# Kernel optimization log

Measured on AMD Instinct MI355X. Metric: run time of the kernel, lower is better.

The kernel has to match this reference:

```python
import jax, jax.numpy as jnp
import numpy as np

ROWS, COLS = 6, 7


def setup_inputs() -> dict:
    key = jax.random.key(0)
    k1, k2 = jax.random.split(key)
    N = 524288
    # gravity-consistent connect-4 boards: each column filled from the bottom
    heights = jax.random.randint(k1, (N, COLS), 0, ROWS + 1)          # pieces per column
    r = jnp.arange(ROWS)[None, :, None]                               # row 0 is top
    filled = r >= (ROWS - heights)[:, None, :]                        # (N, R, C)
    signs = jnp.where(jax.random.bernoulli(k2, 0.5, (N, ROWS, COLS)), 1.0, -1.0)
    x = jnp.where(filled, signs, 0.0).astype(jnp.float32)
    return {"x": x}


def _wins_and_playable(B):
    """For board B (N,R,C) from current player's (+1) perspective, return
    playable (N,C): column not full, and win (N,C): dropping +1 there wins."""
    N = B.shape[0]
    zero = B == 0
    playable = zero[:, 0, :]                                          # (N, C) top cell empty
    rows = jnp.arange(ROWS)
    # landing row = lowest (max-index) empty row per column; -1 if full (masked later)
    land = jnp.max(jnp.where(zero, rows[None, :, None], -1), axis=1)  # (N, C)
    n_idx = jnp.arange(N)[:, None]
    cols = jnp.arange(COLS)[None, :]
    win = jnp.zeros((N, COLS), dtype=bool)
    for dr, dc in ((0, 1), (1, 0), (1, 1), (1, -1)):
        cells = []
        for k in range(-3, 4):
            if k == 0:
                cells.append(jnp.ones((N, COLS), dtype=bool))         # the placed piece itself
                continue
            rr = land + k * dr                                        # (N, C)
            cc = cols + k * dc                                        # (1, C) -> broadcast
            valid = (rr >= 0) & (rr < ROWS) & (cc >= 0) & (cc < COLS)
            v = B[n_idx, jnp.clip(rr, 0, ROWS - 1), jnp.clip(cc, 0, COLS - 1)]
            cells.append(valid & (v == 1.0))
        cells = jnp.stack(cells, axis=-1)                             # (N, C, 7) offsets -3..3
        for s in range(4):                                            # any 4 consecutive
            win = win | jnp.all(cells[..., s:s + 4], axis=-1)
    return playable, win


def reference(x):
    squeeze = x.ndim == 2
    if squeeze:
        x = x[None]
    valids = []
    for sign in (1.0, -1.0):
        playable, win = _wins_and_playable(sign * x)
        valids.append(playable & win)
    valid = jnp.concatenate(valids, axis=1)                           # (N, 2C), priority order
    first = jnp.argmax(valid, axis=1)                                 # first True in scan order
    any_v = jnp.any(valid, axis=1)
    col = first % COLS
    logits = jnp.where(any_v[:, None],
                       jnp.log(jax.nn.one_hot(col, COLS, dtype=jnp.float32) + 1e-12),
                       0.0).astype(jnp.float32)
    return logits[0] if squeeze else logits
```

## Files before the change

kernel.cpp:

```cpp
#include <hip/hip_runtime.h>
#include <stdint.h>

#define THREADS 64
#define BOARDS_PER_BLOCK 128

typedef float f32x4 __attribute__((ext_vector_type(4)));

static constexpr uint64_t colmask(int lo, int hi) {
    uint64_t m = 0;
    for (int r = 0; r < 6; ++r)
        for (int c = lo; c <= hi; ++c)
            m |= 1ull << (7 * r + c);
    return m;
}

static __device__ __forceinline__ uint64_t win_cells(uint64_t P) {
    uint64_t w = 0;
    #pragma unroll
    for (int d = 0; d < 4; ++d) {
        const int s  = (d == 0) ? 1 : (d == 1) ? 7 : (d == 2) ? 8 : 6;
        const int dc = (d == 0) ? 1 : (d == 1) ? 0 : (d == 2) ? 1 : -1;
        const uint64_t M0 = (dc == 0) ? ~0ull : (dc > 0 ? colmask(0, 3) : colmask(3, 6));
        const uint64_t M1 = (dc == 0) ? ~0ull : (dc > 0 ? colmask(1, 4) : colmask(2, 5));
        const uint64_t M2 = (dc == 0) ? ~0ull : (dc > 0 ? colmask(2, 5) : colmask(1, 4));
        const uint64_t M3 = (dc == 0) ? ~0ull : (dc > 0 ? colmask(3, 6) : colmask(0, 3));
        uint64_t r1 = P >> s, r2 = P >> (2 * s), r3 = P >> (3 * s);
        uint64_t l1 = P << s, l2 = P << (2 * s), l3 = P << (3 * s);
        uint64_t u = r1 & r2, v = l1 & l2;
        w |= (u & r3 & M0) | (u & l1 & M1) | (v & r1 & M2) | (v & l3 & M3);
    }
    return w;
}

static __device__ __forceinline__ uint32_t colfold(uint64_t v) {
    v |= v >> 21;
    v |= v >> 7;
    v |= v >> 7;
    return (uint32_t)v & 0x7Fu;
}

extern "C" __global__ void __launch_bounds__(THREADS)
c4_kernel(const float* __restrict__ x, float* __restrict__ out)
{
    __shared__ uint32_t s_pk[BOARDS_PER_BLOCK * 42 / 4];
    __shared__ float    s_out[BOARDS_PER_BLOCK * 7];

    const int tid = threadIdx.x;
    const size_t board0 = (size_t)blockIdx.x * BOARDS_PER_BLOCK;

    const f32x4* src = reinterpret_cast<const f32x4*>(x) + (size_t)blockIdx.x * 1344u;
    #pragma unroll
    for (int k = 0; k < 21; ++k) {
        int n = k * THREADS + tid;
        f32x4 v = __builtin_nontemporal_load(&src[n]);
        uint32_t a = __float_as_uint(v.x), b = __float_as_uint(v.y),
                 c = __float_as_uint(v.z), d = __float_as_uint(v.w);
        uint32_t lo = __builtin_amdgcn_perm(b, a, 0x00000703u) & 0x0000FFFFu;
        uint32_t hi = __builtin_amdgcn_perm(d, c, 0x07030000u) & 0xFFFF0000u;
        s_pk[n] = lo | hi;
    }
    __syncthreads();

    const uint32_t* pk = s_pk + tid * 21;
    uint64_t occ[2] = {0, 0}, MM[2] = {0, 0};
    #pragma unroll
    for (int j = 0; j < 21; ++j) {
        uint32_t e = pk[j];
        uint32_t nO = ((e & 0x20202020u) * 0x00204081u) >> 26;
        uint32_t nM = ((e & 0x80808080u) * 0x00204081u) >> 28;
        if (j < 10) {
            occ[0] |= (uint64_t)nO << (4 * j);
            MM[0]  |= (uint64_t)nM << (4 * j);
        } else if (j == 10) {
            occ[0] |= (uint64_t)(nO & 3u) << 40;
            MM[0]  |= (uint64_t)(nM & 3u) << 40;
            occ[1] |= (uint64_t)(nO >> 2);
            MM[1]  |= (uint64_t)(nM >> 2);
        } else {
            occ[1] |= (uint64_t)nO << (4 * j - 42);
            MM[1]  |= (uint64_t)nM << (4 * j - 42);
        }
    }

    #pragma unroll
    for (int b = 0; b < 2; ++b) {
        uint64_t o = occ[b], m = MM[b], p = o & ~m;
        const uint64_t ROW5 = 0x7Full << 35;
        uint64_t land = ~o & ((o >> 7) | ROW5);

        uint32_t cp = colfold(land & win_cells(p));
        uint32_t cm = colfold(land & win_cells(m));
        uint32_t sel = cp ? cp : cm;
        bool any = (sel != 0u);
        int col  = __ffs(sel) - 1;

        float* so = s_out + (2 * tid + b) * 7;
        #pragma unroll
        for (int c = 0; c < 7; ++c)
            so[c] = (any && c != col) ? -27.631021f : 0.0f;
    }
    __syncthreads();

    float* dst = out + board0 * 7u;
    #pragma unroll
    for (int k = 0; k < 14; ++k) {
        int n = k * THREADS + tid;
        __builtin_nontemporal_store(s_out[n], &dst[n]);
    }
}

extern "C" void kernel_launch(void* const* d_in, const int* in_sizes, int n_in,
                              void* d_out, int out_size, void* d_ws, size_t ws_size,
                              hipStream_t stream)
{
    const float* x = (const float*)d_in[0];
    float* out = (float*)d_out;
    const int N = in_sizes[0] / 42;
    const int grid = N / BOARDS_PER_BLOCK;
    hipLaunchKernelGGL(c4_kernel, dim3(grid), dim3(THREADS), 0, stream, x, out);
}
```

Baseline: 19.34 us.

## Switch to one board per thread with padded 16-bit shared staging

Each thread now handles one board instead of two, in 256-thread blocks of 256 boards. The packed input is written to shared memory as 16-bit halves at a padded per-board stride of 13 dwords, so each thread reads its own board with less bank conflict, and the output buffer reuses the same shared allocation. The win-check builds the board from 32-bit halves rather than 64-bit shifts, aiming to cut register pressure and raise occupancy. In exchange it adds division-by-multiply index math and scattered 16-bit shared stores, plus an extra barrier.

```diff
diff --git a/kernel.cpp b/kernel.cpp
--- a/kernel.cpp
+++ b/kernel.cpp
@@ -1,8 +1,9 @@
 #include <hip/hip_runtime.h>
 #include <stdint.h>
 
-#define THREADS 64
-#define BOARDS_PER_BLOCK 128
+#define THREADS 256
+#define BOARDS_PER_BLOCK 256
+#define STRIDE_DW 13
 
 typedef float f32x4 __attribute__((ext_vector_type(4)));
 
@@ -39,71 +40,71 @@
     return (uint32_t)v & 0x7Fu;
 }
 
-extern "C" __global__ void __launch_bounds__(THREADS)
+extern "C" __global__ void __launch_bounds__(THREADS, 8)
 c4_kernel(const float* __restrict__ x, float* __restrict__ out)
 {
-    __shared__ uint32_t s_pk[BOARDS_PER_BLOCK * 42 / 4];
-    __shared__ float    s_out[BOARDS_PER_BLOCK * 7];
+    __shared__ uint32_t s_mem[BOARDS_PER_BLOCK * STRIDE_DW];
+    uint16_t* s16   = reinterpret_cast<uint16_t*>(s_mem);
+    float*    s_out = reinterpret_cast<float*>(s_mem);
 
     const int tid = threadIdx.x;
     const size_t board0 = (size_t)blockIdx.x * BOARDS_PER_BLOCK;
 
-    const f32x4* src = reinterpret_cast<const f32x4*>(x) + (size_t)blockIdx.x * 1344u;
+    const f32x4* src = reinterpret_cast<const f32x4*>(x) + (size_t)blockIdx.x * 2688u;
     #pragma unroll
-    for (int k = 0; k < 21; ++k) {
+    for (int k = 0; k < 11; ++k) {
         int n = k * THREADS + tid;
-        f32x4 v = __builtin_nontemporal_load(&src[n]);
-        uint32_t a = __float_as_uint(v.x), b = __float_as_uint(v.y),
-                 c = __float_as_uint(v.z), d = __float_as_uint(v.w);
-        uint32_t lo = __builtin_amdgcn_perm(b, a, 0x00000703u) & 0x0000FFFFu;
-        uint32_t hi = __builtin_amdgcn_perm(d, c, 0x07030000u) & 0xFFFF0000u;
-        s_pk[n] = lo | hi;
+        if (n < 2688) {
+            f32x4 v = __builtin_nontemporal_load(&src[n]);
+            uint32_t a = __float_as_uint(v.x), b = __float_as_uint(v.y),
+                     c = __float_as_uint(v.z), d = __float_as_uint(v.w);
+            uint32_t u01 = __builtin_amdgcn_perm(b, a, 0x00000703u);
+            uint32_t u23 = __builtin_amdgcn_perm(d, c, 0x00000703u);
+            uint32_t c0 = 4u * (uint32_t)n;
+            uint32_t b0 = (c0 * 24967u) >> 20;  uint32_t i0 = c0 - 42u * b0;
+            uint32_t c2 = c0 + 2u;
+            uint32_t b2 = (c2 * 24967u) >> 20;  uint32_t i2 = c2 - 42u * b2;
+            s16[26u * b0 + (i0 >> 1)] = (uint16_t)u01;
+            s16[26u * b2 + (i2 >> 1)] = (uint16_t)u23;
+        }
     }
     __syncthreads();
 
-    const uint32_t* pk = s_pk + tid * 21;
-    uint64_t occ[2] = {0, 0}, MM[2] = {0, 0};
+    const uint32_t* pk = s_mem + tid * STRIDE_DW;
+    uint32_t occ_lo = 0, occ_hi = 0, mm_lo = 0, mm_hi = 0;
     #pragma unroll
-    for (int j = 0; j < 21; ++j) {
+    for (int j = 0; j < 11; ++j) {
         uint32_t e = pk[j];
         uint32_t nO = ((e & 0x20202020u) * 0x00204081u) >> 26;
         uint32_t nM = ((e & 0x80808080u) * 0x00204081u) >> 28;
-        if (j < 10) {
-            occ[0] |= (uint64_t)nO << (4 * j);
-            MM[0]  |= (uint64_t)nM << (4 * j);
-        } else if (j == 10) {
-            occ[0] |= (uint64_t)(nO & 3u) << 40;
-            MM[0]  |= (uint64_t)(nM & 3u) << 40;
-            occ[1] |= (uint64_t)(nO >> 2);
-            MM[1]  |= (uint64_t)(nM >> 2);
-        } else {
-            occ[1] |= (uint64_t)nO << (4 * j - 42);
-            MM[1]  |= (uint64_t)nM << (4 * j - 42);
-        }
+        if (j == 10) { nO &= 3u; nM &= 3u; }
+        if (j < 8) { occ_lo |= nO << (4 * j);      mm_lo |= nM << (4 * j); }
+        else       { occ_hi |= nO << (4 * j - 32); mm_hi |= nM << (4 * j - 32); }
     }
+    uint64_t o = (uint64_t)occ_lo | ((uint64_t)occ_hi << 32);
+    uint64_t m = (uint64_t)mm_lo  | ((uint64_t)mm_hi  << 32);
+    uint64_t p = o & ~m;
 
+    const uint64_t ROW5 = 0x7Full << 35;
+    uint64_t land = ~o & ((o >> 7) | ROW5);
+
+    uint32_t cp = colfold(land & win_cells(p));
+    uint32_t cm = colfold(land & win_cells(m));
+    uint32_t sel = cp ? cp : cm;
+    bool any = (sel != 0u);
+    int col  = __ffs(sel) - 1;
+
+    __syncthreads();
+
+    float* so = s_out + tid * 7;
     #pragma unroll
-    for (int b = 0; b < 2; ++b) {
-        uint64_t o = occ[b], m = MM[b], p = o & ~m;
-        const uint64_t ROW5 = 0x7Full << 35;
-        uint64_t land = ~o & ((o >> 7) | ROW5);
-
-        uint32_t cp = colfold(land & win_cells(p));
-        uint32_t cm = colfold(land & win_cells(m));
-        uint32_t sel = cp ? cp : cm;
-        bool any = (sel != 0u);
-        int col  = __ffs(sel) - 1;
-
-        float* so = s_out + (2 * tid + b) * 7;
-        #pragma unroll
-        for (int c = 0; c < 7; ++c)
-            so[c] = (any && c != col) ? -27.631021f : 0.0f;
-    }
+    for (int c = 0; c < 7; ++c)
+        so[c] = (any && c != col) ? -27.631021f : 0.0f;
     __syncthreads();
 
     float* dst = out + board0 * 7u;
     #pragma unroll
-    for (int k = 0; k < 14; ++k) {
+    for (int k = 0; k < 7; ++k) {
         int n = k * THREADS + tid;
         __builtin_nontemporal_store(s_out[n], &dst[n]);
     }
```

Measured after the change: 20.80 us. 1.08x slower.
